# Kernel optimization log

Hardware: AMD Instinct MI355X
Metric: run time of the kernel (lower is better)

The kernel has to match this reference:

```python
import jax, jax.numpy as jnp
from jax import lax
import numpy as np

# LeNet-5 C3 sparse connectivity table (which S2 maps feed each C3 map)
IDX3 = np.array([[0,1,2],[1,2,3],[2,3,4],[3,4,5],[0,4,5],[0,1,5]])            # maps 0-5 (3 inputs)
IDX4 = np.array([[0,1,2,3],[1,2,3,4],[2,3,4,5],[0,3,4,5],[0,1,4,5],
                 [0,1,2,5],[0,1,3,4],[1,2,4,5],[0,2,3,5]])                    # maps 6-14 (4 inputs)


def _conv(x, w):
    return lax.conv_general_dilated(x, w, (1, 1), 'VALID',
                                    dimension_numbers=('NCHW', 'OIHW', 'NCHW'))


def _avgpool2(x):
    s = lax.reduce_window(x, 0.0, lax.add, (1, 1, 2, 2), (1, 1, 2, 2), 'VALID')
    return s * 0.25


def setup_inputs() -> dict:
    key = jax.random.key(0)
    ks = jax.random.split(key, 12)
    f = lambda k, shp: (jax.random.normal(k, shp, dtype=jnp.float32) * 0.1)
    return {
        'x':     jax.random.normal(ks[0], (8192, 1, 32, 32), dtype=jnp.float32),
        'c1_w':  f(ks[1], (6, 1, 5, 5)),   'c1_b': f(ks[2], (6,)),
        'c3_w3': f(ks[3], (6, 3, 5, 5)),   'c3_b3': f(ks[4], (6,)),
        'c3_w4': f(ks[5], (9, 4, 5, 5)),   'c3_b4': f(ks[6], (9,)),
        'c3_w6': f(ks[7], (1, 6, 5, 5)),   'c3_b6': f(ks[8], (1,)),
        'c5_w':  f(ks[9], (120, 16, 5, 5)), 'c5_b': f(ks[10], (120,)),
        'l1_w':  f(ks[11], (84, 120)), 'l1_b': jnp.zeros((84,), jnp.float32),
        'l2_w':  f(jax.random.fold_in(key, 99), (10, 84)), 'l2_b': jnp.zeros((10,), jnp.float32),
    }


def reference(x, c1_w, c1_b, c3_w3, c3_b3, c3_w4, c3_b4, c3_w6, c3_b6,
              c5_w, c5_b, l1_w, l1_b, l2_w, l2_b):
    # C1 + tanh + S2: [B,1,32,32] -> [B,6,14,14]
    out = jnp.tanh(_conv(x, c1_w) + c1_b[None, :, None, None])
    out = _avgpool2(out)

    # C3: fuse the 16 sparse-connectivity convs into one [16,6,5,5] conv
    # by scattering the small per-map kernels into a zero-padded weight.
    W = jnp.zeros((16, 6, 5, 5), dtype=out.dtype)
    W = W.at[np.arange(6)[:, None], IDX3].set(c3_w3)
    W = W.at[np.arange(6, 15)[:, None], IDX4].set(c3_w4)
    W = W.at[15].set(c3_w6[0])
    b = jnp.concatenate([c3_b3, c3_b4, c3_b6])
    out = _conv(out, W) + b[None, :, None, None]          # [B,16,10,10]

    out = _avgpool2(jnp.tanh(out))                        # [B,16,5,5]
    out = _conv(out, c5_w) + c5_b[None, :, None, None]    # [B,120,1,1]
    out = jnp.tanh(out[:, :, 0, 0])                       # [B,120]
    out = jnp.tanh(out @ l1_w.T + l1_b)                   # [B,84]
    return out @ l2_w.T + l2_b                            # [B,10]
```

## Files before the change

kernel.cpp:

```cpp
#include <hip/hip_runtime.h>

typedef float v2f   __attribute__((ext_vector_type(2)));
typedef float f32x4 __attribute__((ext_vector_type(4)));
typedef _Float16 h16;
typedef h16 half8 __attribute__((ext_vector_type(8)));

__device__ __forceinline__ float fast_tanh(float x) {
    float e = __expf(2.0f * x);
    return fmaf(-2.0f, __builtin_amdgcn_rcpf(e + 1.0f), 1.0f);
}
__device__ __forceinline__ v2f fma2(v2f a, v2f b, v2f c) {
    return __builtin_elementwise_fma(a, b, c);
}
__device__ __forceinline__ half8 cvt8(float4 u0, float4 u1) {
    return (half8){(h16)u0.x,(h16)u0.y,(h16)u0.z,(h16)u0.w,
                   (h16)u1.x,(h16)u1.y,(h16)u1.z,(h16)u1.w};
}

#define K1_IMG 4
#define XSTR  34
#define XIMG  (32 * XSTR)
#define K1_SMEM (K1_IMG * XIMG + 192 + 8)

__global__ __launch_bounds__(256) void k_c1(
    const float* __restrict__ x, const float* __restrict__ c1_w,
    const float* __restrict__ c1_b, h16* __restrict__ s2g, int B)
{
    __shared__ __align__(16) float smem[K1_SMEM];
    float* x_s   = smem;
    float* c1w_s = smem + K1_IMG * XIMG;
    float* c1b_s = c1w_s + 192;

    const int tid  = threadIdx.x;
    const int img0 = blockIdx.x * K1_IMG;
    const int nimg = min(K1_IMG, B - img0);
    if (nimg <= 0) return;

    if (tid < 192) {
        int c = tid >> 5, r = tid & 31;
        int row = r / 6, v = r % 6;
        c1w_s[tid] = (row < 5 && v < 5) ? c1_w[c * 25 + row * 5 + v] : 0.0f;
    }
    if (tid < 6) c1b_s[tid] = c1_b[tid];

    {
        const float4* xg = (const float4*)(x + (size_t)img0 * 1024);
        const int n4 = nimg * 256;
        for (int i = tid; i < n4; i += 256) {
            float4 v = xg[i];
            int img = i >> 8, q = i & 255;
            int row = q >> 3, col4 = (q & 7) << 2;
            float* p = x_s + img * XIMG + row * XSTR + col4;
            *(float2*)(p)     = (float2){v.x, v.y};
            *(float2*)(p + 2) = (float2){v.z, v.w};
        }
    }
    __syncthreads();

    for (int it = tid; it < nimg * 168; it += 256) {
        int h   = it & 1;
        int t2  = it >> 1;
        int i   = t2 % 14;
        int t3  = t2 / 14;
        int c   = t3 % 6;
        int img = t3 / 6;
        const float* xb = x_s + img * XIMG + 14 * h;
        const float* wb = c1w_s + c * 32;
        v2f acc2[14];
        #pragma unroll
        for (int j = 0; j < 14; ++j) acc2[j] = (v2f){0.0f, 0.0f};
        float wlo[5], whi[5];
        #pragma unroll
        for (int v = 0; v < 5; ++v) whi[v] = 0.0f;
        #pragma unroll
        for (int xr = 0; xr < 6; ++xr) {
            if (xr <= 4) {
                float2 w0 = *(const float2*)(wb + xr * 6);
                float2 w1 = *(const float2*)(wb + xr * 6 + 2);
                float2 w2 = *(const float2*)(wb + xr * 6 + 4);
                wlo[0] = w0.x; wlo[1] = w0.y; wlo[2] = w1.x; wlo[3] = w1.y; wlo[4] = w2.x;
            } else {
                #pragma unroll
                for (int v = 0; v < 5; ++v) wlo[v] = 0.0f;
            }
            float row[18];
            const float* rp = xb + (2 * i + xr) * XSTR;
            #pragma unroll
            for (int k = 0; k < 9; ++k) {
                float2 t = *(const float2*)(rp + 2 * k);
                row[2 * k] = t.x; row[2 * k + 1] = t.y;
            }
            v2f wp[5];
            #pragma unroll
            for (int v = 0; v < 5; ++v) wp[v] = (v2f){wlo[v], whi[v]};
            #pragma unroll
            for (int j = 0; j < 14; ++j) {
                acc2[j] = fma2((v2f){row[j],     row[j]},     wp[0], acc2[j]);
                acc2[j] = fma2((v2f){row[j + 1], row[j + 1]}, wp[1], acc2[j]);
                acc2[j] = fma2((v2f){row[j + 2], row[j + 2]}, wp[2], acc2[j]);
                acc2[j] = fma2((v2f){row[j + 3], row[j + 3]}, wp[3], acc2[j]);
                acc2[j] = fma2((v2f){row[j + 4], row[j + 4]}, wp[4], acc2[j]);
            }
            #pragma unroll
            for (int v = 0; v < 5; ++v) whi[v] = wlo[v];
        }
        const float b = c1b_s[c];
        h16* o = s2g + (size_t)(img0 + img) * 1176 + c * 196 + i * 14 + 7 * h;
        #pragma unroll
        for (int j = 0; j < 7; ++j) {
            float t00 = fast_tanh(acc2[2 * j].x     + b);
            float t01 = fast_tanh(acc2[2 * j + 1].x + b);
            float t10 = fast_tanh(acc2[2 * j].y     + b);
            float t11 = fast_tanh(acc2[2 * j + 1].y + b);
            o[j] = (h16)(0.25f * (t00 + t01 + t10 + t11));
        }
    }
}

#define S2IMGH 1576
#define C3B_HALVES 3584

__device__ __constant__ int C3_INV[16][6] = {
    {0,1,2,-1,-1,-1},{-1,0,1,2,-1,-1},{-1,-1,0,1,2,-1},{-1,-1,-1,0,1,2},
    {0,-1,-1,-1,1,2},{0,1,-1,-1,-1,2},
    {0,1,2,3,-1,-1},{-1,0,1,2,3,-1},{-1,-1,0,1,2,3},{0,-1,-1,1,2,3},
    {0,1,-1,-1,2,3},{0,1,2,-1,-1,3},{0,1,-1,2,3,-1},{-1,0,1,-1,2,3},
    {0,-1,1,2,-1,3},
    {0,1,2,3,4,5}
};

#define K2_SMEM_BYTES (16 * S2IMGH * 2 + C3B_HALVES * 2 + 64)

__global__ __launch_bounds__(256) void k_c3(
    const h16* __restrict__ s2g,
    const float* __restrict__ c3_w3, const float* __restrict__ c3_b3,
    const float* __restrict__ c3_w4, const float* __restrict__ c3_b4,
    const float* __restrict__ c3_w6, const float* __restrict__ c3_b6,
    h16* __restrict__ s4g, int B)
{
    __shared__ __align__(16) char smem[K2_SMEM_BYTES];
    h16*   s2i   = (h16*)smem;
    h16*   c3Bh  = (h16*)(smem + 16 * S2IMGH * 2);
    float* c3b_s = (float*)(smem + 16 * S2IMGH * 2 + C3B_HALVES * 2);

    const int tid  = threadIdx.x;
    const int img0 = blockIdx.x * 16;
    const int nimg = min(16, B - img0);
    if (nimg <= 0) return;

    {
        float4 z = {0.f, 0.f, 0.f, 0.f};
        float4* zp = (float4*)s2i;
        for (int i = tid; i < 16 * S2IMGH / 8; i += 256) zp[i] = z;
    }
    __syncthreads();

    {
        const int nh2 = nimg * 588;
        for (int idx = tid; idx < nh2; idx += 256) {
            int img = idx / 588, ii = idx % 588;
            int c = ii / 98, p2 = (ii % 98) * 2;
            const h16* g = s2g + (size_t)(img0 + img) * 1176 + c * 196 + p2;
            h16 v0 = g[0], v1 = g[1];
            s2i[img * S2IMGH + p2 * 8 + c]       = v0;
            s2i[img * S2IMGH + (p2 + 1) * 8 + c] = v1;
        }
    }
    #pragma unroll
    for (int u = 0; u < 14; ++u) {
        const int e = tid + 256 * u;
        const int t = e >> 9, rem = e & 511, L = rem >> 3, c = rem & 7;
        const int n = L & 15, chunk = L >> 4;
        int dr, dc; bool valid = true;
        if (t <= 4)      { dr = chunk; dc = t; }
        else if (t == 5) { dr = 4; dc = chunk; }
        else             { dr = 4; dc = 4; valid = (chunk == 0); }
        float val = 0.0f;
        if (valid && c < 6) {
            const int cc = C3_INV[n][c];
            if (cc >= 0) {
                const int off = dr * 5 + dc;
                if (n < 6)       val = c3_w3[(n * 3 + cc) * 25 + off];
                else if (n < 15) val = c3_w4[((n - 6) * 4 + cc) * 25 + off];
                else             val = c3_w6[cc * 25 + off];
            }
        }
        c3Bh[e] = (h16)val;
    }
    if (tid < 6)        c3b_s[tid] = c3_b3[tid];
    else if (tid < 15)  c3b_s[tid] = c3_b4[tid - 6];
    else if (tid == 15) c3b_s[15]  = c3_b6[0];
    __syncthreads();

    {
        const int lane = tid & 63, wv = tid >> 6;
        const int nloc = lane & 15, q4 = lane >> 4;
        half8 bf[7];
        #pragma unroll
        for (int t = 0; t < 7; ++t)
            bf[t] = *(const half8*)(c3Bh + t * 512 + lane * 8);
        const float bias = c3b_s[nloc];
        const int abase = nloc * S2IMGH;
        for (int q = wv; q < 25; q += 4) {
            const int pr = q / 5, pc = q % 5;
            f32x4 acc[2][2];
            #pragma unroll
            for (int a = 0; a < 2; ++a)
                #pragma unroll
                for (int b2 = 0; b2 < 2; ++b2)
                    acc[a][b2] = (f32x4){0.f, 0.f, 0.f, 0.f};
            #pragma unroll
            for (int a = 0; a < 2; ++a) {
                #pragma unroll
                for (int b2 = 0; b2 < 2; ++b2) {
                    const int r = 2 * pr + a, col = 2 * pc + b2;
                    #pragma unroll
                    for (int t = 0; t < 5; ++t) {
                        half8 A = *(const half8*)(s2i + abase + ((r + q4) * 14 + col + t) * 8);
                        acc[a][b2] = __builtin_amdgcn_mfma_f32_16x16x32_f16(A, bf[t], acc[a][b2], 0, 0, 0);
                    }
                    half8 A5 = *(const half8*)(s2i + abase + ((r + 4) * 14 + col + q4) * 8);
                    acc[a][b2] = __builtin_amdgcn_mfma_f32_16x16x32_f16(A5, bf[5], acc[a][b2], 0, 0, 0);
                    half8 A6 = *(const half8*)(s2i + abase + ((r + 4) * 14 + col + 4) * 8);
                    acc[a][b2] = __builtin_amdgcn_mfma_f32_16x16x32_f16(A6, bf[6], acc[a][b2], 0, 0, 0);
                }
            }
            const int pos = pr * 5 + pc;
            #pragma unroll
            for (int rr = 0; rr < 4; ++rr) {
                const int img = q4 * 4 + rr;
                if (img < nimg) {
                    float s = fast_tanh(acc[0][0][rr] + bias) + fast_tanh(acc[0][1][rr] + bias)
                            + fast_tanh(acc[1][0][rr] + bias) + fast_tanh(acc[1][1][rr] + bias);
                    s4g[(size_t)(img0 + img) * 400 + nloc * 25 + pos] = (h16)(0.25f * s);
                }
            }
        }
    }
}

#define KT_IMG   16
#define S4L_STR  424
#define C5O_STR  136
#define F6L_STR  104
#define KT_S4L   0
#define KT_C5OL  (KT_IMG * S4L_STR * 2)
#define KT_F6L   (KT_C5OL + KT_IMG * C5O_STR * 2)
#define KT_BIAS  (KT_F6L + KT_IMG * F6L_STR * 2)
#define KT_SMEM  (KT_BIAS + 240 * 4)

__global__ __launch_bounds__(256) void k_tail(
    const h16* __restrict__ s4g,
    const float* __restrict__ c5_w, const float* __restrict__ c5_b,
    const float* __restrict__ l1_w, const float* __restrict__ l1_b,
    const float* __restrict__ l2_w, const float* __restrict__ l2_b,
    float* __restrict__ out, int B)
{
    __shared__ __align__(16) char smem[KT_SMEM];
    h16*   s4l   = (h16*)(smem + KT_S4L);
    h16*   c5ol  = (h16*)(smem + KT_C5OL);
    h16*   f6l   = (h16*)(smem + KT_F6L);
    float* c5b_s = (float*)(smem + KT_BIAS);
    float* l1b_s = c5b_s + 128;
    float* l2b_s = l1b_s + 96;

    const int tid  = threadIdx.x;
    const int img0 = blockIdx.x * KT_IMG;
    const int nimg = min(KT_IMG, B - img0);
    if (nimg <= 0) return;

    if (tid < 128)      c5b_s[tid] = (tid < 120) ? c5_b[tid] : 0.f;
    else if (tid < 224) { int i = tid - 128; l1b_s[i] = (i < 84) ? l1_b[i] : 0.f; }
    else if (tid < 240) { int i = tid - 224; l2b_s[i] = (i < 10) ? l2_b[i] : 0.f; }

    {
        const half8 z = {(h16)0,(h16)0,(h16)0,(h16)0,(h16)0,(h16)0,(h16)0,(h16)0};
        for (int i = tid; i < KT_IMG * 53; i += 256) {
            int img = i / 53, cc = i % 53;
            half8 v = z;
            if (img < nimg && cc < 50)
                v = *(const half8*)(s4g + (size_t)(img0 + img) * 400 + cc * 8);
            *(half8*)(s4l + img * S4L_STR + cc * 8) = v;
        }
    }
    __syncthreads();

    const int lane = tid & 63, wv = tid >> 6;
    const int nloc = lane & 15, q4 = lane >> 4;
    const half8 z8 = {(h16)0,(h16)0,(h16)0,(h16)0,(h16)0,(h16)0,(h16)0,(h16)0};

    {
        const int nb = wv * 2;
        f32x4 acc[2];
        acc[0] = (f32x4){0.f,0.f,0.f,0.f};
        acc[1] = (f32x4){0.f,0.f,0.f,0.f};
        for (int ks = 0; ks < 13; ++ks) {
            const int ka = ks * 32 + q4 * 8;
            half8 A = *(const half8*)(s4l + nloc * S4L_STR + ka);
            #pragma unroll
            for (int t = 0; t < 2; ++t) {
                const int n = (nb + t) * 16 + nloc;
                half8 Bf = z8;
                if (n < 120 && ka < 400) {
                    float4 u0 = *(const float4*)(c5_w + n * 400 + ka);
                    float4 u1 = *(const float4*)(c5_w + n * 400 + ka + 4);
                    Bf = cvt8(u0, u1);
                }
                acc[t] = __builtin_amdgcn_mfma_f32_16x16x32_f16(A, Bf, acc[t], 0, 0, 0);
            }
        }
        #pragma unroll
        for (int t = 0; t < 2; ++t) {
            const int o = (nb + t) * 16 + nloc;
            const float bo = c5b_s[o];
            #pragma unroll
            for (int r = 0; r < 4; ++r) {
                const int img = q4 * 4 + r;
                c5ol[img * C5O_STR + o] = (h16)fast_tanh(acc[t][r] + bo);
            }
        }
    }
    __syncthreads();

    if (wv < 3) {
        const int nb = wv * 2;
        f32x4 acc[2];
        acc[0] = (f32x4){0.f,0.f,0.f,0.f};
        acc[1] = (f32x4){0.f,0.f,0.f,0.f};
        for (int ks = 0; ks < 4; ++ks) {
            const int ka = ks * 32 + q4 * 8;
            half8 A = *(const half8*)(c5ol + nloc * C5O_STR + ka);
            #pragma unroll
            for (int t = 0; t < 2; ++t) {
                const int n = (nb + t) * 16 + nloc;
                half8 Bf = z8;
                if (n < 84 && ka < 120) {
                    float4 u0 = *(const float4*)(l1_w + n * 120 + ka);
                    float4 u1 = *(const float4*)(l1_w + n * 120 + ka + 4);
                    Bf = cvt8(u0, u1);
                }
                acc[t] = __builtin_amdgcn_mfma_f32_16x16x32_f16(A, Bf, acc[t], 0, 0, 0);
            }
        }
        #pragma unroll
        for (int t = 0; t < 2; ++t) {
            const int o = (nb + t) * 16 + nloc;
            const float bo = l1b_s[o];
            #pragma unroll
            for (int r = 0; r < 4; ++r) {
                const int img = q4 * 4 + r;
                f6l[img * F6L_STR + o] = (h16)fast_tanh(acc[t][r] + bo);
            }
        }
    }
    __syncthreads();

    if (wv == 0) {
        f32x4 acc = (f32x4){0.f,0.f,0.f,0.f};
        #pragma unroll
        for (int ks = 0; ks < 3; ++ks) {
            const int ka = ks * 32 + q4 * 8;
            half8 A = *(const half8*)(f6l + nloc * F6L_STR + ka);
            half8 Bf = z8;
            #pragma unroll
            for (int i = 0; i < 8; ++i) {
                const int k = ka + i;
                if (nloc < 10 && k < 84) Bf[i] = (h16)l2_w[nloc * 84 + k];
            }
            acc = __builtin_amdgcn_mfma_f32_16x16x32_f16(A, Bf, acc, 0, 0, 0);
        }
        if (nloc < 10) {
            #pragma unroll
            for (int r = 0; r < 4; ++r) {
                const int img = q4 * 4 + r;
                if (img < nimg)
                    out[(size_t)(img0 + img) * 10 + nloc] = acc[r] + l2b_s[nloc];
            }
        }
    }
}

extern "C" void kernel_launch(void* const* d_in, const int* in_sizes, int n_in,
                              void* d_out, int out_size, void* d_ws, size_t ws_size,
                              hipStream_t stream) {
    const float* x     = (const float*)d_in[0];
    const float* c1_w  = (const float*)d_in[1];
    const float* c1_b  = (const float*)d_in[2];
    const float* c3_w3 = (const float*)d_in[3];
    const float* c3_b3 = (const float*)d_in[4];
    const float* c3_w4 = (const float*)d_in[5];
    const float* c3_b4 = (const float*)d_in[6];
    const float* c3_w6 = (const float*)d_in[7];
    const float* c3_b6 = (const float*)d_in[8];
    const float* c5_w  = (const float*)d_in[9];
    const float* c5_b  = (const float*)d_in[10];
    const float* l1_w  = (const float*)d_in[11];
    const float* l1_b  = (const float*)d_in[12];
    const float* l2_w  = (const float*)d_in[13];
    const float* l2_b  = (const float*)d_in[14];
    float* out = (float*)d_out;

    const int B = in_sizes[0] / 1024;

    h16* s2g = (h16*)d_ws;
    h16* s4g = (h16*)((char*)d_ws + (size_t)B * 1176 * 2);

    k_c1<<<(B + K1_IMG - 1) / K1_IMG, 256, 0, stream>>>(x, c1_w, c1_b, s2g, B);
    k_c3<<<(B + 15) / 16, 256, 0, stream>>>(s2g, c3_w3, c3_b3, c3_w4, c3_b4,
                                            c3_w6, c3_b6, s4g, B);
    k_tail<<<(B + KT_IMG - 1) / KT_IMG, 256, 0, stream>>>(s4g, c5_w, c5_b,
                                                          l1_w, l1_b, l2_w, l2_b, out, B);
}
```

Before: 182.5 us.

## Compute C1 convolution with fp16 MFMA and write S2 in C3's padded layout

Replaces the scalar packed-FMA C1 convolution with 16x16x32 fp16 MFMA instructions, using Toeplitz-style weight fragments in registers and a sliding window of input rows held in half precision in LDS. Tanh and 2x2 average pooling are fused into the MFMA epilogue via a lane shuffle. S2 is written directly in the channel-interleaved padded layout that C3 expects, so C3 can load it with plain vector copies instead of zeroing and scattering. Input is rounded to fp16 before the convolution, which lowers accuracy, and the workspace per image grows. The S2 padding region is no longer zeroed in global memory, so C3 depends on that padding never being read.

```diff
diff --git a/kernel.cpp b/kernel.cpp
--- a/kernel.cpp
+++ b/kernel.cpp
@@ -4,44 +4,38 @@
 typedef float f32x4 __attribute__((ext_vector_type(4)));
 typedef _Float16 h16;
 typedef h16 half8 __attribute__((ext_vector_type(8)));
+typedef h16 half4 __attribute__((ext_vector_type(4)));
 
 __device__ __forceinline__ float fast_tanh(float x) {
     float e = __expf(2.0f * x);
     return fmaf(-2.0f, __builtin_amdgcn_rcpf(e + 1.0f), 1.0f);
 }
-__device__ __forceinline__ v2f fma2(v2f a, v2f b, v2f c) {
-    return __builtin_elementwise_fma(a, b, c);
-}
 __device__ __forceinline__ half8 cvt8(float4 u0, float4 u1) {
     return (half8){(h16)u0.x,(h16)u0.y,(h16)u0.z,(h16)u0.w,
                    (h16)u1.x,(h16)u1.y,(h16)u1.z,(h16)u1.w};
 }
 
-#define K1_IMG 4
-#define XSTR  34
-#define XIMG  (32 * XSTR)
-#define K1_SMEM (K1_IMG * XIMG + 192 + 8)
+#define S2IMGH 1576
+
+#define C1_IMG 8
+#define XROW  40
+#define XIMGH (32 * XROW + 8)
 
 __global__ __launch_bounds__(256) void k_c1(
     const float* __restrict__ x, const float* __restrict__ c1_w,
     const float* __restrict__ c1_b, h16* __restrict__ s2g, int B)
 {
-    __shared__ __align__(16) float smem[K1_SMEM];
-    float* x_s   = smem;
-    float* c1w_s = smem + K1_IMG * XIMG;
-    float* c1b_s = c1w_s + 192;
+    __shared__ __align__(16) h16 xs[C1_IMG * XIMGH];
+    __shared__ float c1w_s[152];
+    __shared__ float c1b_s[8];
 
     const int tid  = threadIdx.x;
-    const int img0 = blockIdx.x * K1_IMG;
-    const int nimg = min(K1_IMG, B - img0);
+    const int img0 = blockIdx.x * C1_IMG;
+    const int nimg = min(C1_IMG, B - img0);
     if (nimg <= 0) return;
 
-    if (tid < 192) {
-        int c = tid >> 5, r = tid & 31;
-        int row = r / 6, v = r % 6;
-        c1w_s[tid] = (row < 5 && v < 5) ? c1_w[c * 25 + row * 5 + v] : 0.0f;
-    }
-    if (tid < 6) c1b_s[tid] = c1_b[tid];
+    if (tid < 150) c1w_s[tid] = c1_w[tid];
+    if (tid < 6)   c1b_s[tid] = c1_b[tid];
 
     {
         const float4* xg = (const float4*)(x + (size_t)img0 * 1024);
@@ -50,74 +44,83 @@
             float4 v = xg[i];
             int img = i >> 8, q = i & 255;
             int row = q >> 3, col4 = (q & 7) << 2;
-            float* p = x_s + img * XIMG + row * XSTR + col4;
-            *(float2*)(p)     = (float2){v.x, v.y};
-            *(float2*)(p + 2) = (float2){v.z, v.w};
+            *(half4*)(xs + img * XIMGH + row * XROW + col4) =
+                (half4){(h16)v.x, (h16)v.y, (h16)v.z, (h16)v.w};
         }
     }
     __syncthreads();
 
-    for (int it = tid; it < nimg * 168; it += 256) {
-        int h   = it & 1;
-        int t2  = it >> 1;
-        int i   = t2 % 14;
-        int t3  = t2 / 14;
-        int c   = t3 % 6;
-        int img = t3 / 6;
-        const float* xb = x_s + img * XIMG + 14 * h;
-        const float* wb = c1w_s + c * 32;
-        v2f acc2[14];
-        #pragma unroll
-        for (int j = 0; j < 14; ++j) acc2[j] = (v2f){0.0f, 0.0f};
-        float wlo[5], whi[5];
-        #pragma unroll
-        for (int v = 0; v < 5; ++v) whi[v] = 0.0f;
-        #pragma unroll
-        for (int xr = 0; xr < 6; ++xr) {
-            if (xr <= 4) {
-                float2 w0 = *(const float2*)(wb + xr * 6);
-                float2 w1 = *(const float2*)(wb + xr * 6 + 2);
-                float2 w2 = *(const float2*)(wb + xr * 6 + 4);
-                wlo[0] = w0.x; wlo[1] = w0.y; wlo[2] = w1.x; wlo[3] = w1.y; wlo[4] = w2.x;
-            } else {
+    const int lane = tid & 63, wv = tid >> 6;
+    const int nloc = lane & 15, q4 = lane >> 4;
+
+    half8 bf[3][5];
+    float bias[3];
+    #pragma unroll
+    for (int t = 0; t < 3; ++t) {
+        const int tile = 3 * wv + t;
+        const int map  = tile >> 1;
+        const int j    = ((tile & 1) << 4) + nloc;
+        bias[t] = c1b_s[map];
+        #pragma unroll
+        for (int ks = 0; ks < 5; ++ks) {
+            half8 f;
+            #pragma unroll
+            for (int jj = 0; jj < 8; ++jj) {
+                const int d = q4 * 8 + jj - j;
+                f[jj] = (d >= 0 && d < 5) ? (h16)c1w_s[map * 25 + ks * 5 + d] : (h16)0;
+            }
+            bf[t][ks] = f;
+        }
+    }
+
+    const int imgL = nloc >> 1, hf = nloc & 1;
+    const h16* xrow = xs + imgL * XIMGH + hf * (14 * XROW) + q4 * 8;
+    half8 rf[5];
+    #pragma unroll
+    for (int r = 0; r < 5; ++r) rf[r] = *(const half8*)(xrow + r * XROW);
+
+    float t0[3][4];
+    for (int cr = 0; cr < 14; ++cr) {
+        f32x4 acc[3];
+        #pragma unroll
+        for (int t = 0; t < 3; ++t) acc[t] = (f32x4){0.f, 0.f, 0.f, 0.f};
+        #pragma unroll
+        for (int ks = 0; ks < 5; ++ks) {
+            #pragma unroll
+            for (int t = 0; t < 3; ++t)
+                acc[t] = __builtin_amdgcn_mfma_f32_16x16x32_f16(rf[ks], bf[t][ks], acc[t], 0, 0, 0);
+        }
+        if ((cr & 1) == 0) {
+            #pragma unroll
+            for (int t = 0; t < 3; ++t)
                 #pragma unroll
-                for (int v = 0; v < 5; ++v) wlo[v] = 0.0f;
-            }
-            float row[18];
-            const float* rp = xb + (2 * i + xr) * XSTR;
-            #pragma unroll
-            for (int k = 0; k < 9; ++k) {
-                float2 t = *(const float2*)(rp + 2 * k);
-                row[2 * k] = t.x; row[2 * k + 1] = t.y;
-            }
-            v2f wp[5];
-            #pragma unroll
-            for (int v = 0; v < 5; ++v) wp[v] = (v2f){wlo[v], whi[v]};
-            #pragma unroll
-            for (int j = 0; j < 14; ++j) {
-                acc2[j] = fma2((v2f){row[j],     row[j]},     wp[0], acc2[j]);
-                acc2[j] = fma2((v2f){row[j + 1], row[j + 1]}, wp[1], acc2[j]);
-                acc2[j] = fma2((v2f){row[j + 2], row[j + 2]}, wp[2], acc2[j]);
-                acc2[j] = fma2((v2f){row[j + 3], row[j + 3]}, wp[3], acc2[j]);
-                acc2[j] = fma2((v2f){row[j + 4], row[j + 4]}, wp[4], acc2[j]);
-            }
-            #pragma unroll
-            for (int v = 0; v < 5; ++v) whi[v] = wlo[v];
-        }
-        const float b = c1b_s[c];
-        h16* o = s2g + (size_t)(img0 + img) * 1176 + c * 196 + i * 14 + 7 * h;
-        #pragma unroll
-        for (int j = 0; j < 7; ++j) {
-            float t00 = fast_tanh(acc2[2 * j].x     + b);
-            float t01 = fast_tanh(acc2[2 * j + 1].x + b);
-            float t10 = fast_tanh(acc2[2 * j].y     + b);
-            float t11 = fast_tanh(acc2[2 * j + 1].y + b);
-            o[j] = (h16)(0.25f * (t00 + t01 + t10 + t11));
-        }
-    }
-}
-
-#define S2IMGH 1576
+                for (int r = 0; r < 4; ++r)
+                    t0[t][r] = fast_tanh(acc[t][r] + bias[t]);
+        } else {
+            #pragma unroll
+            for (int t = 0; t < 3; ++t) {
+                const int tile = 3 * wv + t;
+                const int jp   = (((tile & 1) << 4) + nloc) >> 1;
+                const int map  = tile >> 1;
+                #pragma unroll
+                for (int r = 0; r < 4; ++r) {
+                    float s = t0[t][r] + fast_tanh(acc[t][r] + bias[t]);
+                    float o = 0.25f * (s + __shfl_xor(s, 1));
+                    const int m = q4 * 4 + r;
+                    const int img = m >> 1, mh = m & 1;
+                    const int ip  = (cr >> 1) + 7 * mh;
+                    if (!(lane & 1) && jp < 14 && img < nimg)
+                        s2g[(size_t)(img0 + img) * S2IMGH + (ip * 14 + jp) * 8 + map] = (h16)o;
+                }
+            }
+        }
+        if (cr < 13) {
+            rf[0] = rf[1]; rf[1] = rf[2]; rf[2] = rf[3]; rf[3] = rf[4];
+            rf[4] = *(const half8*)(xrow + (cr + 5) * XROW);
+        }
+    }
+}
+
 #define C3B_HALVES 3584
 
 __device__ __constant__ int C3_INV[16][6] = {
@@ -149,21 +152,11 @@
     if (nimg <= 0) return;
 
     {
-        float4 z = {0.f, 0.f, 0.f, 0.f};
-        float4* zp = (float4*)s2i;
-        for (int i = tid; i < 16 * S2IMGH / 8; i += 256) zp[i] = z;
-    }
-    __syncthreads();
-
-    {
-        const int nh2 = nimg * 588;
-        for (int idx = tid; idx < nh2; idx += 256) {
-            int img = idx / 588, ii = idx % 588;
-            int c = ii / 98, p2 = (ii % 98) * 2;
-            const h16* g = s2g + (size_t)(img0 + img) * 1176 + c * 196 + p2;
-            h16 v0 = g[0], v1 = g[1];
-            s2i[img * S2IMGH + p2 * 8 + c]       = v0;
-            s2i[img * S2IMGH + (p2 + 1) * 8 + c] = v1;
+        const int img = tid >> 4;
+        if (img < nimg) {
+            for (int c = (tid & 15); c < 197; c += 16)
+                *(half8*)(s2i + img * S2IMGH + c * 8) =
+                    *(const half8*)(s2g + (size_t)(img0 + img) * S2IMGH + c * 8);
         }
     }
     #pragma unroll
@@ -403,9 +396,9 @@
     const int B = in_sizes[0] / 1024;
 
     h16* s2g = (h16*)d_ws;
-    h16* s4g = (h16*)((char*)d_ws + (size_t)B * 1176 * 2);
-
-    k_c1<<<(B + K1_IMG - 1) / K1_IMG, 256, 0, stream>>>(x, c1_w, c1_b, s2g, B);
+    h16* s4g = (h16*)((char*)d_ws + (size_t)B * S2IMGH * 2);
+
+    k_c1<<<(B + C1_IMG - 1) / C1_IMG, 256, 0, stream>>>(x, c1_w, c1_b, s2g, B);
     k_c3<<<(B + 15) / 16, 256, 0, stream>>>(s2g, c3_w3, c3_b3, c3_w4, c3_b4,
                                             c3_w6, c3_b6, s4g, B);
     k_tail<<<(B + KT_IMG - 1) / KT_IMG, 256, 0, stream>>>(s4g, c5_w, c5_b,
```

After: 178.6 us. -2.1%, faster.
